# Performance work log

Measured on AMD Instinct MI355X. Metric: run time of the kernel, lower is better.

The kernel has to match this reference:

```python
import jax, jax.numpy as jnp
import numpy as np

NUM_RNA = 1927
N_NODES = 100000
N_EDGES = 1600000
IN_C, HID_C, OUT_C = 128, 128, 64
EPS = 1e-5  # BatchNorm1d default eps


def gcn_conv(x, W, b, src, dst, num_nodes):
    """PyG GCNConv: linear transform, add self-loops, symmetric-normalized scatter-add."""
    h = x @ W  # [N, C_out]
    loop = jnp.arange(num_nodes, dtype=src.dtype)
    s = jnp.concatenate([src, loop])  # self-loops appended
    d = jnp.concatenate([dst, loop])
    deg = jax.ops.segment_sum(jnp.ones(d.shape[0], dtype=h.dtype), d, num_segments=num_nodes)
    dinv = jnp.where(deg > 0, jax.lax.rsqrt(deg), jnp.zeros_like(deg))
    norm = dinv[s] * dinv[d]  # [E+N]
    msg = h[s] * norm[:, None]  # [E+N, C_out] gather (memory-bound)
    out = jax.ops.segment_sum(msg, d, num_segments=num_nodes)  # scatter-add
    return out + b


def batchnorm(x, gamma, beta):
    # training-mode BatchNorm1d: batch stats over node dim, biased variance
    mu = jnp.mean(x, axis=0)
    var = jnp.mean(jnp.square(x - mu), axis=0)
    return (x - mu) * jax.lax.rsqrt(var + EPS) * gamma + beta


def setup_inputs() -> dict:
    key = jax.random.key(0)
    ks = jax.random.split(key, 6)
    x = jax.random.normal(ks[0], (N_NODES, IN_C), dtype=jnp.float32)
    edge_index = jax.random.randint(ks[1], (2, N_EDGES), 0, N_NODES)
    # xavier_uniform for conv weights
    lim1 = float(np.sqrt(6.0 / (IN_C + HID_C)))
    lim2 = float(np.sqrt(6.0 / (HID_C + OUT_C)))
    W1 = jax.random.uniform(ks[2], (IN_C, HID_C), minval=-lim1, maxval=lim1, dtype=jnp.float32)
    W2 = jax.random.uniform(ks[3], (HID_C, OUT_C), minval=-lim2, maxval=lim2, dtype=jnp.float32)
    b1 = jnp.zeros((HID_C,), dtype=jnp.float32)
    b2 = jnp.zeros((OUT_C,), dtype=jnp.float32)
    gamma1 = jnp.ones((HID_C,), dtype=jnp.float32)
    beta1 = jnp.zeros((HID_C,), dtype=jnp.float32)
    gamma2 = jnp.ones((OUT_C,), dtype=jnp.float32)
    beta2 = jnp.zeros((OUT_C,), dtype=jnp.float32)
    return {"x": x, "edge_index": edge_index, "W1": W1, "b1": b1,
            "gamma1": gamma1, "beta1": beta1, "W2": W2, "b2": b2,
            "gamma2": gamma2, "beta2": beta2}


def reference(x, edge_index, W1, b1, gamma1, beta1, W2, b2, gamma2, beta2):
    src, dst = edge_index[0], edge_index[1]
    h = gcn_conv(x, W1, b1, src, dst, N_NODES)
    h = jax.nn.relu(batchnorm(h, gamma1, beta1))
    h = gcn_conv(h, W2, b2, src, dst, N_NODES)
    h = batchnorm(h, gamma2, beta2)
    return h[:NUM_RNA], h[NUM_RNA:]
```

## Files before the change

kernel.cpp:

```cpp
#include <hip/hip_runtime.h>
#include <hip/hip_bf16.h>


#define IN_C 128
#define HID_C 128
#define OUT_C2 64
#define BN_EPS 1e-5f
#define NB_STATS 1024
#define NSLAB 64

typedef __attribute__((ext_vector_type(8))) short short8v;
typedef __attribute__((ext_vector_type(4))) float float4v;
typedef __attribute__((ext_vector_type(4))) int int4v;

__device__ inline ushort f2bf(float f) {
    union { float f; unsigned u; } x; x.f = f;
    return (ushort)((x.u + 0x7fffu + ((x.u >> 16) & 1u)) >> 16);
}
__device__ inline float bf2f(ushort u) {
    union { unsigned u; float f; } x; x.u = ((unsigned)u) << 16;
    return x.f;
}

__global__ void init_kernel(float* __restrict__ ws, int n) {
    int i = blockIdx.x * blockDim.x + threadIdx.x;
    if (i < n) ws[i] = 0.0f;
}

template <int OC>
__device__ inline void wreorder_impl(const float* __restrict__ W,
                                     ushort* __restrict__ wfrag, int t) {
    constexpr int NCT = OC / 16;
    int lane = t & 63;
    int rest = t >> 6;
    int ct = rest % NCT;
    int kk = rest / NCT;
    int col = ct * 16 + (lane & 15);
    int krow = kk * 32 + (lane >> 4) * 8;
    ushort tmp[8];
    #pragma unroll
    for (int e = 0; e < 8; ++e)
        tmp[e] = f2bf(W[(size_t)(krow + e) * OC + col]);
    uint4 st;
    st.x = (uint)tmp[0] | ((uint)tmp[1] << 16);
    st.y = (uint)tmp[2] | ((uint)tmp[3] << 16);
    st.z = (uint)tmp[4] | ((uint)tmp[5] << 16);
    st.w = (uint)tmp[6] | ((uint)tmp[7] << 16);
    *(uint4*)&wfrag[(size_t)t * 8] = st;
}

__global__ __launch_bounds__(256) void bucket_count_kernel(
    const int* __restrict__ dst, int* __restrict__ bcnt, int E, int nbA,
    const float* __restrict__ W1, const float* __restrict__ W2,
    ushort* __restrict__ wf1, ushort* __restrict__ wf2)
{
    if (blockIdx.x >= nbA) {
        int b = blockIdx.x - nbA;
        if (b < 8) wreorder_impl<HID_C>(W1, wf1, b * 256 + threadIdx.x);
        else       wreorder_impl<OUT_C2>(W2, wf2, (b - 8) * 256 + threadIdx.x);
        return;
    }
    __shared__ int h[512];
    int t = threadIdx.x;
    h[t] = 0; h[t + 256] = 0;
    __syncthreads();
    int i0 = blockIdx.x * 1024 + t * 4;
    if (i0 < E) {
        int4v d = __builtin_nontemporal_load((const int4v*)&dst[i0]);
        atomicAdd(&h[d.x >> 8], 1);
        atomicAdd(&h[d.y >> 8], 1);
        atomicAdd(&h[d.z >> 8], 1);
        atomicAdd(&h[d.w >> 8], 1);
    }
    __syncthreads();
    if (h[t])       atomicAdd(&bcnt[t], h[t]);
    if (h[t + 256]) atomicAdd(&bcnt[t + 256], h[t + 256]);
}

__global__ __launch_bounds__(256) void bucket_scatter_kernel(
    const int* __restrict__ src, const int* __restrict__ dst,
    const int* __restrict__ bcnt, int* __restrict__ bcursor,
    int2* __restrict__ pairs, int E)
{
    __shared__ int bs[512];
    __shared__ int h[512];
    __shared__ int gb[512];
    int t = threadIdx.x;
    int a = bcnt[t], b = bcnt[t + 256];
    bs[t] = a; bs[t + 256] = b;
    __syncthreads();
    for (int off = 1; off < 512; off <<= 1) {
        int v0 = (t >= off) ? bs[t - off] : 0;
        int v1 = bs[t + 256 - off];
        __syncthreads();
        bs[t] += v0; bs[t + 256] += v1;
        __syncthreads();
    }
    int e0 = bs[t] - a, e1 = bs[t + 256] - b;
    __syncthreads();
    bs[t] = e0; bs[t + 256] = e1;
    h[t] = 0; h[t + 256] = 0;
    __syncthreads();
    int i0 = blockIdx.x * 1024 + t * 4;
    bool act = i0 < E;
    int4v d, s;
    int bk0 = 0, bk1 = 0, bk2 = 0, bk3 = 0, r0 = 0, r1 = 0, r2 = 0, r3 = 0;
    if (act) {
        d = __builtin_nontemporal_load((const int4v*)&dst[i0]);
        s = __builtin_nontemporal_load((const int4v*)&src[i0]);
        bk0 = d.x >> 8; r0 = atomicAdd(&h[bk0], 1);
        bk1 = d.y >> 8; r1 = atomicAdd(&h[bk1], 1);
        bk2 = d.z >> 8; r2 = atomicAdd(&h[bk2], 1);
        bk3 = d.w >> 8; r3 = atomicAdd(&h[bk3], 1);
    }
    __syncthreads();
    if (h[t])       gb[t] = bs[t] + atomicAdd(&bcursor[t], h[t]);
    if (h[t + 256]) gb[t + 256] = bs[t + 256] + atomicAdd(&bcursor[t + 256], h[t + 256]);
    __syncthreads();
    if (act) {
        pairs[gb[bk0] + r0] = make_int2(s.x, d.x);
        pairs[gb[bk1] + r1] = make_int2(s.y, d.y);
        pairs[gb[bk2] + r2] = make_int2(s.z, d.z);
        pairs[gb[bk3] + r3] = make_int2(s.w, d.w);
    }
}

__global__ __launch_bounds__(256) void bucket_csr_kernel(
    const int2* __restrict__ pairs, const int* __restrict__ bcnt,
    int* __restrict__ csr_src, int* __restrict__ row_ptr,
    float* __restrict__ dinv, int E, int N)
{
    __shared__ int bs[512];
    __shared__ int cnt[256];
    __shared__ int sd[256];
    int t = threadIdx.x;
    int a = bcnt[t], b = bcnt[t + 256];
    bs[t] = a; bs[t + 256] = b;
    __syncthreads();
    for (int off = 1; off < 512; off <<= 1) {
        int v0 = (t >= off) ? bs[t - off] : 0;
        int v1 = bs[t + 256 - off];
        __syncthreads();
        bs[t] += v0; bs[t + 256] += v1;
        __syncthreads();
    }
    int e0 = bs[t] - a, e1 = bs[t + 256] - b;
    __syncthreads();
    bs[t] = e0; bs[t + 256] = e1;
    __syncthreads();
    int node0 = blockIdx.x << 8;
    int base = bs[blockIdx.x];
    int end  = (blockIdx.x == 511) ? E : bs[blockIdx.x + 1];
    if (blockIdx.x == 0 && t == 0) row_ptr[N] = E;
    cnt[t] = 0;
    __syncthreads();
    for (int i = base + t; i < end; i += 256)
        atomicAdd(&cnt[pairs[i].y & 255], 1);
    __syncthreads();
    int myc = cnt[t];
    sd[t] = myc;
    __syncthreads();
    for (int off = 1; off < 256; off <<= 1) {
        int v = (t >= off) ? sd[t - off] : 0;
        __syncthreads();
        sd[t] += v;
        __syncthreads();
    }
    int ofs = sd[t] - myc;
    int node = node0 + t;
    if (node < N) {
        row_ptr[node] = base + ofs;
        dinv[node] = rsqrtf((float)myc + 1.0f);
    }
    cnt[t] = ofs;
    __syncthreads();
    for (int i = base + t; i < end; i += 256) {
        int2 p = pairs[i];
        int pos = atomicAdd(&cnt[p.y & 255], 1);
        csr_src[base + pos] = p.x;
    }
}

template <int OC, bool BN_IN>
__global__ __launch_bounds__(256) void mfma_gemm_kernel(
    const void* __restrict__ Xv, const ushort* __restrict__ wfrag,
    ushort* __restrict__ Y, const float* __restrict__ dinv,
    const float* __restrict__ sc, const float* __restrict__ sh, int N)
{
    constexpr int NCT = OC / 16;
    int wave = (blockIdx.x * 256 + threadIdx.x) >> 6;
    int lane = threadIdx.x & 63;
    int row16 = wave * 16;
    if (row16 >= N) return;
    int r = lane & 15;
    int g = lane >> 4;
    int row = row16 + r;

    float4v acc[NCT];
    #pragma unroll
    for (int ct = 0; ct < NCT; ++ct) acc[ct] = (float4v){0.f, 0.f, 0.f, 0.f};

    const short8v* wf = (const short8v*)wfrag;

    #pragma unroll
    for (int kk = 0; kk < 4; ++kk) {
        int k0 = kk * 32 + g * 8;
        short8v a;
        if constexpr (!BN_IN) {
            const float* xp = (const float*)Xv + (size_t)row * 128 + k0;
            float4v x0 = __builtin_nontemporal_load((const float4v*)xp);
            float4v x1 = __builtin_nontemporal_load((const float4v*)(xp + 4));
            a[0] = (short)f2bf(x0[0]); a[1] = (short)f2bf(x0[1]);
            a[2] = (short)f2bf(x0[2]); a[3] = (short)f2bf(x0[3]);
            a[4] = (short)f2bf(x1[0]); a[5] = (short)f2bf(x1[1]);
            a[6] = (short)f2bf(x1[2]); a[7] = (short)f2bf(x1[3]);
        } else {
            const ushort* xp = (const ushort*)Xv + (size_t)row * 128 + k0;
            uint4 v = *(const uint4*)xp;
            float4 s0 = *(const float4*)&sc[k0];
            float4 s1 = *(const float4*)&sc[k0 + 4];
            float4 h0 = *(const float4*)&sh[k0];
            float4 h1 = *(const float4*)&sh[k0 + 4];
            a[0] = (short)f2bf(fmaxf(fmaf(bf2f((ushort)(v.x & 0xffff)), s0.x, h0.x), 0.f));
            a[1] = (short)f2bf(fmaxf(fmaf(bf2f((ushort)(v.x >> 16)),    s0.y, h0.y), 0.f));
            a[2] = (short)f2bf(fmaxf(fmaf(bf2f((ushort)(v.y & 0xffff)), s0.z, h0.z), 0.f));
            a[3] = (short)f2bf(fmaxf(fmaf(bf2f((ushort)(v.y >> 16)),    s0.w, h0.w), 0.f));
            a[4] = (short)f2bf(fmaxf(fmaf(bf2f((ushort)(v.z & 0xffff)), s1.x, h1.x), 0.f));
            a[5] = (short)f2bf(fmaxf(fmaf(bf2f((ushort)(v.z >> 16)),    s1.y, h1.y), 0.f));
            a[6] = (short)f2bf(fmaxf(fmaf(bf2f((ushort)(v.w & 0xffff)), s1.z, h1.z), 0.f));
            a[7] = (short)f2bf(fmaxf(fmaf(bf2f((ushort)(v.w >> 16)),    s1.w, h1.w), 0.f));
        }
        #pragma unroll
        for (int ct = 0; ct < NCT; ++ct) {
            short8v b = wf[((size_t)(kk * NCT + ct)) * 64 + lane];
            acc[ct] = __builtin_amdgcn_mfma_f32_16x16x32_bf16(a, b, acc[ct], 0, 0, 0);
        }
    }
    float di[4];
    #pragma unroll
    for (int i = 0; i < 4; ++i) di[i] = dinv[row16 + g * 4 + i];
    #pragma unroll
    for (int ct = 0; ct < NCT; ++ct) {
        #pragma unroll
        for (int i = 0; i < 4; ++i) {
            int orow = row16 + g * 4 + i;
            Y[(size_t)orow * OC + ct * 16 + r] = f2bf(acc[ct][i] * di[i]);
        }
    }
}

template <int C>
__global__ __launch_bounds__(256) void aggregate_kernel(
    const ushort* __restrict__ h, const int* __restrict__ row_ptr,
    const int* __restrict__ csr_src, const float* __restrict__ dinv,
    ushort* __restrict__ out, int N)
{
    constexpr int TPN = C / 8;
    constexpr int PAR = 64 / TPN;
    int wid = (blockIdx.x * 256 + threadIdx.x) >> 6;
    if (wid >= N) return;
    int lane = threadIdx.x & 63;
    int part = lane / TPN;
    int c0 = (lane % TPN) * 8;
    float acc[8] = {0.f, 0.f, 0.f, 0.f, 0.f, 0.f, 0.f, 0.f};

    uint4 vself = make_uint4(0u, 0u, 0u, 0u);
    if (part == 0) vself = *(const uint4*)&h[(size_t)wid * C + c0];

    int e = row_ptr[wid] + part;
    int e1 = row_ptr[wid + 1];
    for (; e + PAR < e1; e += 2 * PAR) {
        int s0 = __builtin_nontemporal_load(&csr_src[e]);
        int s1 = __builtin_nontemporal_load(&csr_src[e + PAR]);
        uint4 v0 = *(const uint4*)&h[(size_t)s0 * C + c0];
        uint4 v1 = *(const uint4*)&h[(size_t)s1 * C + c0];
        acc[0] += bf2f((ushort)(v0.x & 0xffff)) + bf2f((ushort)(v1.x & 0xffff));
        acc[1] += bf2f((ushort)(v0.x >> 16))    + bf2f((ushort)(v1.x >> 16));
        acc[2] += bf2f((ushort)(v0.y & 0xffff)) + bf2f((ushort)(v1.y & 0xffff));
        acc[3] += bf2f((ushort)(v0.y >> 16))    + bf2f((ushort)(v1.y >> 16));
        acc[4] += bf2f((ushort)(v0.z & 0xffff)) + bf2f((ushort)(v1.z & 0xffff));
        acc[5] += bf2f((ushort)(v0.z >> 16))    + bf2f((ushort)(v1.z >> 16));
        acc[6] += bf2f((ushort)(v0.w & 0xffff)) + bf2f((ushort)(v1.w & 0xffff));
        acc[7] += bf2f((ushort)(v0.w >> 16))    + bf2f((ushort)(v1.w >> 16));
    }
    if (e < e1) {
        int s = __builtin_nontemporal_load(&csr_src[e]);
        uint4 v = *(const uint4*)&h[(size_t)s * C + c0];
        acc[0] += bf2f((ushort)(v.x & 0xffff));
        acc[1] += bf2f((ushort)(v.x >> 16));
        acc[2] += bf2f((ushort)(v.y & 0xffff));
        acc[3] += bf2f((ushort)(v.y >> 16));
        acc[4] += bf2f((ushort)(v.z & 0xffff));
        acc[5] += bf2f((ushort)(v.z >> 16));
        acc[6] += bf2f((ushort)(v.w & 0xffff));
        acc[7] += bf2f((ushort)(v.w >> 16));
    }
    if (part == 0) {
        acc[0] += bf2f((ushort)(vself.x & 0xffff));
        acc[1] += bf2f((ushort)(vself.x >> 16));
        acc[2] += bf2f((ushort)(vself.y & 0xffff));
        acc[3] += bf2f((ushort)(vself.y >> 16));
        acc[4] += bf2f((ushort)(vself.z & 0xffff));
        acc[5] += bf2f((ushort)(vself.z >> 16));
        acc[6] += bf2f((ushort)(vself.w & 0xffff));
        acc[7] += bf2f((ushort)(vself.w >> 16));
    }
    #pragma unroll
    for (int off = TPN; off < 64; off <<= 1) {
        #pragma unroll
        for (int j = 0; j < 8; ++j)
            acc[j] += __shfl_xor(acc[j], off, 64);
    }
    if (part == 0) {
        float dd = dinv[wid];
        uint4 st;
        #pragma unroll
        for (int j = 0; j < 8; ++j) acc[j] *= dd;
        st.x = (uint)f2bf(acc[0]) | ((uint)f2bf(acc[1]) << 16);
        st.y = (uint)f2bf(acc[2]) | ((uint)f2bf(acc[3]) << 16);
        st.z = (uint)f2bf(acc[4]) | ((uint)f2bf(acc[5]) << 16);
        st.w = (uint)f2bf(acc[6]) | ((uint)f2bf(acc[7]) << 16);
        *(uint4*)&out[(size_t)wid * C + c0] = st;
    }
}

template <int C>
__global__ __launch_bounds__(256) void stats_prep_kernel(
    const ushort* __restrict__ h, float* __restrict__ sums,
    const float* __restrict__ gamma, const float* __restrict__ beta,
    float* __restrict__ sc, float* __restrict__ sh,
    int* __restrict__ ticket, int nblocks, int N)
{
    constexpr int CG = C / 8;
    constexpr int RPB = 256 / CG;
    __shared__ float red[RPB][CG][16];
    __shared__ bool lastblk;
    int tid = threadIdx.x;
    int cg = tid % CG, rg = tid / CG;
    int c0 = cg * 8;
    float s[8] = {0.f,0.f,0.f,0.f,0.f,0.f,0.f,0.f};
    float q[8] = {0.f,0.f,0.f,0.f,0.f,0.f,0.f,0.f};
    for (int r = blockIdx.x * RPB + rg; r < N; r += gridDim.x * RPB) {
        uint4 v = *(const uint4*)&h[(size_t)r * C + c0];
        float f0 = bf2f((ushort)(v.x & 0xffff)), f1 = bf2f((ushort)(v.x >> 16));
        float f2 = bf2f((ushort)(v.y & 0xffff)), f3 = bf2f((ushort)(v.y >> 16));
        float f4 = bf2f((ushort)(v.z & 0xffff)), f5 = bf2f((ushort)(v.z >> 16));
        float f6 = bf2f((ushort)(v.w & 0xffff)), f7 = bf2f((ushort)(v.w >> 16));
        s[0]+=f0; s[1]+=f1; s[2]+=f2; s[3]+=f3; s[4]+=f4; s[5]+=f5; s[6]+=f6; s[7]+=f7;
        q[0]=fmaf(f0,f0,q[0]); q[1]=fmaf(f1,f1,q[1]); q[2]=fmaf(f2,f2,q[2]); q[3]=fmaf(f3,f3,q[3]);
        q[4]=fmaf(f4,f4,q[4]); q[5]=fmaf(f5,f5,q[5]); q[6]=fmaf(f6,f6,q[6]); q[7]=fmaf(f7,f7,q[7]);
    }
    #pragma unroll
    for (int j = 0; j < 8; ++j) { red[rg][cg][j] = s[j]; red[rg][cg][8 + j] = q[j]; }
    __syncthreads();
    float* slab = sums + (size_t)(blockIdx.x & (NSLAB - 1)) * 2 * C;
    if (rg == 0) {
        float a[16];
        #pragma unroll
        for (int i = 0; i < 16; ++i) a[i] = red[0][cg][i];
        for (int r2 = 1; r2 < RPB; ++r2)
            #pragma unroll
            for (int i = 0; i < 16; ++i) a[i] += red[r2][cg][i];
        #pragma unroll
        for (int j = 0; j < 8; ++j) {
            atomicAdd(&slab[c0 + j], a[j]);
            atomicAdd(&slab[C + c0 + j], a[8 + j]);
        }
    }
    __syncthreads();
    if (tid == 0) {
        __threadfence();
        int old = atomicAdd(ticket, 1);
        lastblk = (old == nblocks - 1);
    }
    __syncthreads();
    if (lastblk && tid < C) {
        float sv = 0.f, qv = 0.f;
        #pragma unroll 4
        for (int k = 0; k < NSLAB; ++k) {
            sv += atomicAdd(&sums[(size_t)k * 2 * C + tid], 0.0f);
            qv += atomicAdd(&sums[(size_t)k * 2 * C + C + tid], 0.0f);
        }
        float invN = 1.0f / (float)N;
        float mu = sv * invN;
        float var = qv * invN - mu * mu;
        float scl = rsqrtf(var + BN_EPS) * gamma[tid];
        sc[tid] = scl;
        sh[tid] = beta[tid] - mu * scl;
    }
}

__global__ void bn_apply_kernel(const ushort* __restrict__ in, float* __restrict__ out,
                                const float* __restrict__ sc, const float* __restrict__ sh,
                                int N)
{
    int total = N * (OUT_C2 / 8);
    int i = blockIdx.x * blockDim.x + threadIdx.x;
    int stride = gridDim.x * blockDim.x;
    for (; i < total; i += stride) {
        int c0 = (i & 7) * 8;
        uint4 v = *(const uint4*)&in[(size_t)i * 8];
        float4 s0 = *(const float4*)&sc[c0];
        float4 s1 = *(const float4*)&sc[c0 + 4];
        float4 h0 = *(const float4*)&sh[c0];
        float4 h1 = *(const float4*)&sh[c0 + 4];
        float4 o0, o1;
        o0.x = fmaf(bf2f((ushort)(v.x & 0xffff)), s0.x, h0.x);
        o0.y = fmaf(bf2f((ushort)(v.x >> 16)),    s0.y, h0.y);
        o0.z = fmaf(bf2f((ushort)(v.y & 0xffff)), s0.z, h0.z);
        o0.w = fmaf(bf2f((ushort)(v.y >> 16)),    s0.w, h0.w);
        o1.x = fmaf(bf2f((ushort)(v.z & 0xffff)), s1.x, h1.x);
        o1.y = fmaf(bf2f((ushort)(v.z >> 16)),    s1.y, h1.y);
        o1.z = fmaf(bf2f((ushort)(v.w & 0xffff)), s1.z, h1.z);
        o1.w = fmaf(bf2f((ushort)(v.w >> 16)),    s1.w, h1.w);
        *(float4*)&out[(size_t)i * 8] = o0;
        *(float4*)&out[(size_t)i * 8 + 4] = o1;
    }
}

extern "C" void kernel_launch(void* const* d_in, const int* in_sizes, int n_in,
                              void* d_out, int out_size, void* d_ws, size_t ws_size,
                              hipStream_t stream) {
    const float* x      = (const float*)d_in[0];
    const int*   ei     = (const int*)d_in[1];
    const float* W1     = (const float*)d_in[2];
    const float* gamma1 = (const float*)d_in[4];
    const float* beta1  = (const float*)d_in[5];
    const float* W2     = (const float*)d_in[6];
    const float* gamma2 = (const float*)d_in[8];
    const float* beta2  = (const float*)d_in[9];

    const int N = in_sizes[0] / IN_C;
    const int E = in_sizes[1] / 2;
    const int* src = ei;
    const int* dst = ei + E;
    const int nbA   = (E + 1023) / 1024;
    const int nbuck = (N + 255) >> 8;

    float* ws      = (float*)d_ws;
    float* stats1  = ws;
    float* stats2  = ws + 16384;
    float* sc1     = ws + 24576;
    float* sh1     = ws + 24704;
    float* sc2     = ws + 24832;
    float* sh2     = ws + 24896;
    int*   ticket1 = (int*)(ws + 24960);
    int*   ticket2 = (int*)(ws + 24961);
    int*   bcnt    = (int*)(ws + 24976);
    int*   bcursor = (int*)(ws + 25488);
    float* dinv    = ws + 26000;
    int*   row_ptr = (int*)(dinv + N);
    int*   csr_src = row_ptr + N + 16;
    ushort* wfrag1 = (ushort*)(csr_src + E);
    ushort* wfrag2 = wfrag1 + 16384;
    ushort* h1     = wfrag2 + 8192;
    ushort* bufB   = h1 + (size_t)N * HID_C;
    ushort* h2     = bufB + (size_t)N * HID_C;
    ushort* agg2b  = h2 + (size_t)N * OUT_C2;
    int2*  pairs   = (int2*)h2;

    const int nbGemm = (N / 16 + 3) / 4;
    const int initN = 26000;

    init_kernel<<<(initN + 255) / 256, 256, 0, stream>>>(ws, initN);
    bucket_count_kernel<<<nbA + 12, 256, 0, stream>>>(dst, bcnt, E, nbA,
                                                      W1, W2, wfrag1, wfrag2);
    bucket_scatter_kernel<<<nbA, 256, 0, stream>>>(src, dst, bcnt, bcursor, pairs, E);
    bucket_csr_kernel<<<nbuck, 256, 0, stream>>>(pairs, bcnt, csr_src, row_ptr,
                                                 dinv, E, N);

    mfma_gemm_kernel<HID_C, false><<<nbGemm, 256, 0, stream>>>(
        x, wfrag1, h1, dinv, nullptr, nullptr, N);
    aggregate_kernel<HID_C><<<(N + 3) / 4, 256, 0, stream>>>(
        h1, row_ptr, csr_src, dinv, bufB, N);
    stats_prep_kernel<HID_C><<<NB_STATS, 256, 0, stream>>>(
        bufB, stats1, gamma1, beta1, sc1, sh1, ticket1, NB_STATS, N);

    mfma_gemm_kernel<OUT_C2, true><<<nbGemm, 256, 0, stream>>>(
        bufB, wfrag2, h2, dinv, sc1, sh1, N);
    aggregate_kernel<OUT_C2><<<(N + 3) / 4, 256, 0, stream>>>(
        h2, row_ptr, csr_src, dinv, agg2b, N);
    stats_prep_kernel<OUT_C2><<<NB_STATS, 256, 0, stream>>>(
        agg2b, stats2, gamma2, beta2, sc2, sh2, ticket2, NB_STATS, N);

    bn_apply_kernel<<<2048, 256, 0, stream>>>(agg2b, (float*)d_out, sc2, sh2, N);
}
```

Baseline: 333.8 us.

## Fuse CSR preprocessing and first GEMM into one persistent kernel with grid barriers

Replaces the init, bucket count, bucket scatter, CSR build and first GEMM launches with one persistent kernel of 1024 blocks that synchronises its phases through atomic-counter grid barriers. Workspace zeroing moves to hipMemsetAsync. The aim is to remove several kernel launch gaps and tail effects. In exchange, the grid barrier assumes all 1024 blocks are co-resident (launch bounds 256,4), spin-waiting adds latency, and the count and scatter phases now run fewer blocks that each loop over tiles.

```diff
diff --git a/kernel.cpp b/kernel.cpp
--- a/kernel.cpp
+++ b/kernel.cpp
@@ -8,6 +8,7 @@
 #define BN_EPS 1e-5f
 #define NB_STATS 1024
 #define NSLAB 64
+#define NB_PRE 1024
 
 typedef __attribute__((ext_vector_type(8))) short short8v;
 typedef __attribute__((ext_vector_type(4))) float float4v;
@@ -22,9 +23,14 @@
     return x.f;
 }
 
-__global__ void init_kernel(float* __restrict__ ws, int n) {
-    int i = blockIdx.x * blockDim.x + threadIdx.x;
-    if (i < n) ws[i] = 0.0f;
+__device__ inline void gbar(int* ctr, int target) {
+    __syncthreads();
+    if (threadIdx.x == 0) {
+        __threadfence();
+        atomicAdd(ctr, 1);
+        while (atomicAdd(ctr, 0) < target) __builtin_amdgcn_s_sleep(8);
+    }
+    __syncthreads();
 }
 
 template <int OC>
@@ -49,147 +55,14 @@
     *(uint4*)&wfrag[(size_t)t * 8] = st;
 }
 
-__global__ __launch_bounds__(256) void bucket_count_kernel(
-    const int* __restrict__ dst, int* __restrict__ bcnt, int E, int nbA,
-    const float* __restrict__ W1, const float* __restrict__ W2,
-    ushort* __restrict__ wf1, ushort* __restrict__ wf2)
-{
-    if (blockIdx.x >= nbA) {
-        int b = blockIdx.x - nbA;
-        if (b < 8) wreorder_impl<HID_C>(W1, wf1, b * 256 + threadIdx.x);
-        else       wreorder_impl<OUT_C2>(W2, wf2, (b - 8) * 256 + threadIdx.x);
-        return;
-    }
-    __shared__ int h[512];
-    int t = threadIdx.x;
-    h[t] = 0; h[t + 256] = 0;
-    __syncthreads();
-    int i0 = blockIdx.x * 1024 + t * 4;
-    if (i0 < E) {
-        int4v d = __builtin_nontemporal_load((const int4v*)&dst[i0]);
-        atomicAdd(&h[d.x >> 8], 1);
-        atomicAdd(&h[d.y >> 8], 1);
-        atomicAdd(&h[d.z >> 8], 1);
-        atomicAdd(&h[d.w >> 8], 1);
-    }
-    __syncthreads();
-    if (h[t])       atomicAdd(&bcnt[t], h[t]);
-    if (h[t + 256]) atomicAdd(&bcnt[t + 256], h[t + 256]);
-}
-
-__global__ __launch_bounds__(256) void bucket_scatter_kernel(
-    const int* __restrict__ src, const int* __restrict__ dst,
-    const int* __restrict__ bcnt, int* __restrict__ bcursor,
-    int2* __restrict__ pairs, int E)
-{
-    __shared__ int bs[512];
-    __shared__ int h[512];
-    __shared__ int gb[512];
-    int t = threadIdx.x;
-    int a = bcnt[t], b = bcnt[t + 256];
-    bs[t] = a; bs[t + 256] = b;
-    __syncthreads();
-    for (int off = 1; off < 512; off <<= 1) {
-        int v0 = (t >= off) ? bs[t - off] : 0;
-        int v1 = bs[t + 256 - off];
-        __syncthreads();
-        bs[t] += v0; bs[t + 256] += v1;
-        __syncthreads();
-    }
-    int e0 = bs[t] - a, e1 = bs[t + 256] - b;
-    __syncthreads();
-    bs[t] = e0; bs[t + 256] = e1;
-    h[t] = 0; h[t + 256] = 0;
-    __syncthreads();
-    int i0 = blockIdx.x * 1024 + t * 4;
-    bool act = i0 < E;
-    int4v d, s;
-    int bk0 = 0, bk1 = 0, bk2 = 0, bk3 = 0, r0 = 0, r1 = 0, r2 = 0, r3 = 0;
-    if (act) {
-        d = __builtin_nontemporal_load((const int4v*)&dst[i0]);
-        s = __builtin_nontemporal_load((const int4v*)&src[i0]);
-        bk0 = d.x >> 8; r0 = atomicAdd(&h[bk0], 1);
-        bk1 = d.y >> 8; r1 = atomicAdd(&h[bk1], 1);
-        bk2 = d.z >> 8; r2 = atomicAdd(&h[bk2], 1);
-        bk3 = d.w >> 8; r3 = atomicAdd(&h[bk3], 1);
-    }
-    __syncthreads();
-    if (h[t])       gb[t] = bs[t] + atomicAdd(&bcursor[t], h[t]);
-    if (h[t + 256]) gb[t + 256] = bs[t + 256] + atomicAdd(&bcursor[t + 256], h[t + 256]);
-    __syncthreads();
-    if (act) {
-        pairs[gb[bk0] + r0] = make_int2(s.x, d.x);
-        pairs[gb[bk1] + r1] = make_int2(s.y, d.y);
-        pairs[gb[bk2] + r2] = make_int2(s.z, d.z);
-        pairs[gb[bk3] + r3] = make_int2(s.w, d.w);
-    }
-}
-
-__global__ __launch_bounds__(256) void bucket_csr_kernel(
-    const int2* __restrict__ pairs, const int* __restrict__ bcnt,
-    int* __restrict__ csr_src, int* __restrict__ row_ptr,
-    float* __restrict__ dinv, int E, int N)
-{
-    __shared__ int bs[512];
-    __shared__ int cnt[256];
-    __shared__ int sd[256];
-    int t = threadIdx.x;
-    int a = bcnt[t], b = bcnt[t + 256];
-    bs[t] = a; bs[t + 256] = b;
-    __syncthreads();
-    for (int off = 1; off < 512; off <<= 1) {
-        int v0 = (t >= off) ? bs[t - off] : 0;
-        int v1 = bs[t + 256 - off];
-        __syncthreads();
-        bs[t] += v0; bs[t + 256] += v1;
-        __syncthreads();
-    }
-    int e0 = bs[t] - a, e1 = bs[t + 256] - b;
-    __syncthreads();
-    bs[t] = e0; bs[t + 256] = e1;
-    __syncthreads();
-    int node0 = blockIdx.x << 8;
-    int base = bs[blockIdx.x];
-    int end  = (blockIdx.x == 511) ? E : bs[blockIdx.x + 1];
-    if (blockIdx.x == 0 && t == 0) row_ptr[N] = E;
-    cnt[t] = 0;
-    __syncthreads();
-    for (int i = base + t; i < end; i += 256)
-        atomicAdd(&cnt[pairs[i].y & 255], 1);
-    __syncthreads();
-    int myc = cnt[t];
-    sd[t] = myc;
-    __syncthreads();
-    for (int off = 1; off < 256; off <<= 1) {
-        int v = (t >= off) ? sd[t - off] : 0;
-        __syncthreads();
-        sd[t] += v;
-        __syncthreads();
-    }
-    int ofs = sd[t] - myc;
-    int node = node0 + t;
-    if (node < N) {
-        row_ptr[node] = base + ofs;
-        dinv[node] = rsqrtf((float)myc + 1.0f);
-    }
-    cnt[t] = ofs;
-    __syncthreads();
-    for (int i = base + t; i < end; i += 256) {
-        int2 p = pairs[i];
-        int pos = atomicAdd(&cnt[p.y & 255], 1);
-        csr_src[base + pos] = p.x;
-    }
-}
-
 template <int OC, bool BN_IN>
-__global__ __launch_bounds__(256) void mfma_gemm_kernel(
+__device__ inline void gemm_body(
     const void* __restrict__ Xv, const ushort* __restrict__ wfrag,
     ushort* __restrict__ Y, const float* __restrict__ dinv,
-    const float* __restrict__ sc, const float* __restrict__ sh, int N)
+    const float* __restrict__ sc, const float* __restrict__ sh,
+    int N, int wave, int lane)
 {
     constexpr int NCT = OC / 16;
-    int wave = (blockIdx.x * 256 + threadIdx.x) >> 6;
-    int lane = threadIdx.x & 63;
     int row16 = wave * 16;
     if (row16 >= N) return;
     int r = lane & 15;
@@ -249,6 +122,159 @@
     }
 }
 
+__global__ __launch_bounds__(256, 4) void preproc_gemm1_kernel(
+    const int* __restrict__ src, const int* __restrict__ dst,
+    int* __restrict__ bcnt, int* __restrict__ bcursor, int2* __restrict__ pairs,
+    int* __restrict__ csr_src, int* __restrict__ row_ptr, float* __restrict__ dinv,
+    int* __restrict__ bar,
+    const float* __restrict__ W1, const float* __restrict__ W2,
+    ushort* __restrict__ wf1, ushort* __restrict__ wf2,
+    const float* __restrict__ x, ushort* __restrict__ h1,
+    int E, int N, int nTiles, int nbuck, int nbGemm)
+{
+    __shared__ int smem[1536];
+    int t = threadIdx.x;
+
+    if (blockIdx.x < 12) {
+        if (blockIdx.x < 8) wreorder_impl<HID_C>(W1, wf1, blockIdx.x * 256 + t);
+        else                wreorder_impl<OUT_C2>(W2, wf2, (blockIdx.x - 8) * 256 + t);
+    }
+    {
+        int* h = smem;
+        h[t] = 0; h[t + 256] = 0;
+        __syncthreads();
+        for (int tile = blockIdx.x; tile < nTiles; tile += NB_PRE) {
+            int i0 = tile * 1024 + t * 4;
+            if (i0 < E) {
+                int4v d = __builtin_nontemporal_load((const int4v*)&dst[i0]);
+                atomicAdd(&h[d.x >> 8], 1);
+                atomicAdd(&h[d.y >> 8], 1);
+                atomicAdd(&h[d.z >> 8], 1);
+                atomicAdd(&h[d.w >> 8], 1);
+            }
+        }
+        __syncthreads();
+        if (h[t])       atomicAdd(&bcnt[t], h[t]);
+        if (h[t + 256]) atomicAdd(&bcnt[t + 256], h[t + 256]);
+    }
+    gbar(&bar[0], NB_PRE);
+
+    {
+        int* bs = smem;
+        int* h  = smem + 512;
+        int* gb = smem + 1024;
+        int a = bcnt[t], b = bcnt[t + 256];
+        bs[t] = a; bs[t + 256] = b;
+        __syncthreads();
+        for (int off = 1; off < 512; off <<= 1) {
+            int v0 = (t >= off) ? bs[t - off] : 0;
+            int v1 = bs[t + 256 - off];
+            __syncthreads();
+            bs[t] += v0; bs[t + 256] += v1;
+            __syncthreads();
+        }
+        int e0 = bs[t] - a, e1 = bs[t + 256] - b;
+        __syncthreads();
+        bs[t] = e0; bs[t + 256] = e1;
+        __syncthreads();
+        for (int tile = blockIdx.x; tile < nTiles; tile += NB_PRE) {
+            h[t] = 0; h[t + 256] = 0;
+            __syncthreads();
+            int i0 = tile * 1024 + t * 4;
+            bool act = i0 < E;
+            int4v d, s;
+            int bk0 = 0, bk1 = 0, bk2 = 0, bk3 = 0, r0 = 0, r1 = 0, r2 = 0, r3 = 0;
+            if (act) {
+                d = __builtin_nontemporal_load((const int4v*)&dst[i0]);
+                s = __builtin_nontemporal_load((const int4v*)&src[i0]);
+                bk0 = d.x >> 8; r0 = atomicAdd(&h[bk0], 1);
+                bk1 = d.y >> 8; r1 = atomicAdd(&h[bk1], 1);
+                bk2 = d.z >> 8; r2 = atomicAdd(&h[bk2], 1);
+                bk3 = d.w >> 8; r3 = atomicAdd(&h[bk3], 1);
+            }
+            __syncthreads();
+            if (h[t])       gb[t] = bs[t] + atomicAdd(&bcursor[t], h[t]);
+            if (h[t + 256]) gb[t + 256] = bs[t + 256] + atomicAdd(&bcursor[t + 256], h[t + 256]);
+            __syncthreads();
+            if (act) {
+                pairs[gb[bk0] + r0] = make_int2(s.x, d.x);
+                pairs[gb[bk1] + r1] = make_int2(s.y, d.y);
+                pairs[gb[bk2] + r2] = make_int2(s.z, d.z);
+                pairs[gb[bk3] + r3] = make_int2(s.w, d.w);
+            }
+            __syncthreads();
+        }
+    }
+    gbar(&bar[1], NB_PRE);
+
+    if (blockIdx.x < nbuck) {
+        int* bs  = smem;
+        int* cnt = smem + 512;
+        int* sd  = smem + 768;
+        int a = bcnt[t], b = bcnt[t + 256];
+        bs[t] = a; bs[t + 256] = b;
+        __syncthreads();
+        for (int off = 1; off < 512; off <<= 1) {
+            int v0 = (t >= off) ? bs[t - off] : 0;
+            int v1 = bs[t + 256 - off];
+            __syncthreads();
+            bs[t] += v0; bs[t + 256] += v1;
+            __syncthreads();
+        }
+        int e0 = bs[t] - a, e1 = bs[t + 256] - b;
+        __syncthreads();
+        bs[t] = e0; bs[t + 256] = e1;
+        __syncthreads();
+        int node0 = blockIdx.x << 8;
+        int base = bs[blockIdx.x];
+        int end  = (blockIdx.x == 511) ? E : bs[blockIdx.x + 1];
+        if (blockIdx.x == 0 && t == 0) row_ptr[N] = E;
+        cnt[t] = 0;
+        __syncthreads();
+        for (int i = base + t; i < end; i += 256)
+            atomicAdd(&cnt[pairs[i].y & 255], 1);
+        __syncthreads();
+        int myc = cnt[t];
+        sd[t] = myc;
+        __syncthreads();
+        for (int off = 1; off < 256; off <<= 1) {
+            int v = (t >= off) ? sd[t - off] : 0;
+            __syncthreads();
+            sd[t] += v;
+            __syncthreads();
+        }
+        int ofs = sd[t] - myc;
+        int node = node0 + t;
+        if (node < N) {
+            row_ptr[node] = base + ofs;
+            dinv[node] = rsqrtf((float)myc + 1.0f);
+        }
+        cnt[t] = ofs;
+        __syncthreads();
+        for (int i = base + t; i < end; i += 256) {
+            int2 p = pairs[i];
+            int pos = atomicAdd(&cnt[p.y & 255], 1);
+            csr_src[base + pos] = p.x;
+        }
+    }
+    gbar(&bar[2], NB_PRE);
+
+    int wv = t >> 6, lane = t & 63;
+    for (int tile = blockIdx.x; tile < nbGemm; tile += NB_PRE)
+        gemm_body<HID_C, false>(x, wf1, h1, dinv, nullptr, nullptr,
+                                N, tile * 4 + wv, lane);
+}
+
+template <int OC, bool BN_IN>
+__global__ __launch_bounds__(256) void mfma_gemm_kernel(
+    const void* __restrict__ Xv, const ushort* __restrict__ wfrag,
+    ushort* __restrict__ Y, const float* __restrict__ dinv,
+    const float* __restrict__ sc, const float* __restrict__ sh, int N)
+{
+    int wave = (blockIdx.x * 256 + threadIdx.x) >> 6;
+    gemm_body<OC, BN_IN>(Xv, wfrag, Y, dinv, sc, sh, N, wave, threadIdx.x & 63);
+}
+
 template <int C>
 __global__ __launch_bounds__(256) void aggregate_kernel(
     const ushort* __restrict__ h, const int* __restrict__ row_ptr,
@@ -434,8 +460,8 @@
     const int E = in_sizes[1] / 2;
     const int* src = ei;
     const int* dst = ei + E;
-    const int nbA   = (E + 1023) / 1024;
-    const int nbuck = (N + 255) >> 8;
+    const int nTiles = (E + 1023) / 1024;
+    const int nbuck  = (N + 255) >> 8;
 
     float* ws      = (float*)d_ws;
     float* stats1  = ws;
@@ -446,6 +472,7 @@
     float* sh2     = ws + 24896;
     int*   ticket1 = (int*)(ws + 24960);
     int*   ticket2 = (int*)(ws + 24961);
+    int*   bar     = (int*)(ws + 24964);
     int*   bcnt    = (int*)(ws + 24976);
     int*   bcursor = (int*)(ws + 25488);
     float* dinv    = ws + 26000;
@@ -460,17 +487,13 @@
     int2*  pairs   = (int2*)h2;
 
     const int nbGemm = (N / 16 + 3) / 4;
-    const int initN = 26000;
-
-    init_kernel<<<(initN + 255) / 256, 256, 0, stream>>>(ws, initN);
-    bucket_count_kernel<<<nbA + 12, 256, 0, stream>>>(dst, bcnt, E, nbA,
-                                                      W1, W2, wfrag1, wfrag2);
-    bucket_scatter_kernel<<<nbA, 256, 0, stream>>>(src, dst, bcnt, bcursor, pairs, E);
-    bucket_csr_kernel<<<nbuck, 256, 0, stream>>>(pairs, bcnt, csr_src, row_ptr,
-                                                 dinv, E, N);
-
-    mfma_gemm_kernel<HID_C, false><<<nbGemm, 256, 0, stream>>>(
-        x, wfrag1, h1, dinv, nullptr, nullptr, N);
+
+    hipMemsetAsync(ws, 0, (size_t)26000 * 4, stream);
+
+    preproc_gemm1_kernel<<<NB_PRE, 256, 0, stream>>>(
+        src, dst, bcnt, bcursor, pairs, csr_src, row_ptr, dinv, bar,
+        W1, W2, wfrag1, wfrag2, x, h1, E, N, nTiles, nbuck, nbGemm);
+
     aggregate_kernel<HID_C><<<(N + 3) / 4, 256, 0, stream>>>(
         h1, row_ptr, csr_src, dinv, bufB, N);
     stats_prep_kernel<HID_C><<<NB_STATS, 256, 0, stream>>>(
```

Result: slower. 578.6 us (+73.3%).
